# Kernel optimization log

Hardware: AMD Instinct MI355X
Metric: run time of the kernel (lower is better)

The kernel has to match this reference:

```python
import jax, jax.numpy as jnp
import numpy as np

LAYERS, BLOCKS = 10, 4
NL = LAYERS * BLOCKS
RC, DC, SC, EC, CLASSES, K = 32, 32, 256, 256, 256, 2
B, T = 8, 16384


def setup_inputs() -> dict:
    key = jax.random.key(0)
    ks = jax.random.split(key, 10)
    s = 0.1  # small init so tanh/sigmoid stay in informative range
    f32 = jnp.float32
    return {
        "x": jax.random.normal(ks[0], (B, CLASSES, T), dtype=f32),
        "w_in": jax.random.normal(ks[1], (RC, CLASSES, 1), dtype=f32) * s,
        "b_in": jnp.zeros((RC,), dtype=f32),
        "filt_w": jax.random.normal(ks[2], (NL, DC, RC, K), dtype=f32) * s,
        "filt_b": jnp.zeros((NL, DC), dtype=f32),
        "gate_w": jax.random.normal(ks[3], (NL, DC, RC, K), dtype=f32) * s,
        "gate_b": jnp.zeros((NL, DC), dtype=f32),
        "res_w": jax.random.normal(ks[4], (NL, RC, DC, K), dtype=f32) * s,
        "res_b": jnp.zeros((NL, RC), dtype=f32),
        "skip_w": jax.random.normal(ks[5], (NL, SC, DC, K), dtype=f32) * s,
        "skip_b": jnp.zeros((NL, SC), dtype=f32),
        "end1_w": jax.random.normal(ks[6], (EC, SC, 1), dtype=f32) * s,
        "end1_b": jnp.zeros((EC,), dtype=f32),
        "end2_w": jax.random.normal(ks[7], (CLASSES, EC, 1), dtype=f32) * s,
        "end2_b": jnp.zeros((CLASSES,), dtype=f32),
    }


def _causal_conv(x, w, b, d):
    # Equivalent to torch Conv1d(padding=d, dilation=d, k=2) followed by [:, :, :L]:
    # y[t] = w[..,0] @ x[t-d] + w[..,1] @ x[t]
    y = jax.lax.conv_general_dilated(
        x, w, window_strides=(1,), padding=[(d, 0)], rhs_dilation=(d,),
        dimension_numbers=("NCH", "OIH", "NCH"))
    return y + b[None, :, None]


def _conv1x1(x, w, b):
    return jnp.einsum("bct,oc->bot", x, w[:, :, 0]) + b[None, :, None]


def reference(x, w_in, b_in, filt_w, filt_b, gate_w, gate_b,
              res_w, res_b, skip_w, skip_b, end1_w, end1_b, end2_w, end2_b):
    h = _conv1x1(x, w_in, b_in)                      # [B, RC, T]
    skip = jnp.zeros((x.shape[0], SC, x.shape[2]), dtype=x.dtype)
    for i in range(NL):
        d = 2 ** (i % LAYERS)
        f = jnp.tanh(_causal_conv(h, filt_w[i], filt_b[i], d))
        g = jax.nn.sigmoid(_causal_conv(h, gate_w[i], gate_b[i], d))
        z = f * g                                    # [B, DC, T]
        skip = skip + _causal_conv(z, skip_w[i], skip_b[i], d)
        h = h + _causal_conv(z, res_w[i], res_b[i], d)
    out = jax.nn.relu(skip)
    out = jax.nn.relu(_conv1x1(out, end1_w, end1_b))
    out = _conv1x1(out, end2_w, end2_b)              # [B, CLASSES, T]
    n, c, l = out.shape
    return out.transpose(0, 2, 1).reshape(n * l, c)  # [B*T, CLASSES]
```

## Files before the change

### kernel.cpp

```cpp
#include <hip/hip_runtime.h>
#include <cstdint>
#include <cstddef>

#define T_LEN    16384
#define BATCH    8
#define BT       (BATCH * T_LEN)
#define NLAYERS  40

typedef unsigned short ushort_t;
typedef unsigned int   uint_t;
typedef __attribute__((ext_vector_type(8))) short    short8;
typedef __attribute__((ext_vector_type(4))) float    float4v;
typedef __attribute__((ext_vector_type(8))) _Float16 half8;

__device__ __forceinline__ ushort_t f2bf(float f) {
    union { float f; uint_t i; } v; v.f = f;
    uint_t r = (v.i + 0x7FFFu + ((v.i >> 16) & 1u)) >> 16;
    return (ushort_t)r;
}
__device__ __forceinline__ float fast_rcp(float x) {
#if __has_builtin(__builtin_amdgcn_rcpf)
    return __builtin_amdgcn_rcpf(x);
#else
    return 1.f / x;
#endif
}
__device__ __forceinline__ float tanh_fast(float x) {
    float e = __expf(2.f * x);
    return 1.f - 2.f * fast_rcp(e + 1.f);
}
__device__ __forceinline__ float sigmoid_fast(float x) {
    return fast_rcp(1.f + __expf(-x));
}
__device__ __forceinline__ float4v mfma16(short8 a, short8 b, float4v c) {
    return __builtin_amdgcn_mfma_f32_16x16x32_bf16(a, b, c, 0, 0, 0);
}

__global__ __launch_bounds__(256) void k_prep(
    const float* __restrict__ filt_w, const float* __restrict__ gate_w,
    const float* __restrict__ res_w,  const float* __restrict__ skip_w,
    const float* __restrict__ end1_w, const float* __restrict__ end2_w,
    const float* __restrict__ filt_b, const float* __restrict__ gate_b,
    const float* __restrict__ res_b,  const float* __restrict__ skip_b,
    const float* __restrict__ end1_b, const float* __restrict__ end2_b,
    ushort_t* __restrict__ wfgF, ushort_t* __restrict__ wrF,
    ushort_t* __restrict__ bsF,  ushort_t* __restrict__ e1F, ushort_t* __restrict__ e2F,
    float* __restrict__ bfg, float* __restrict__ brb, float* __restrict__ bsum,
    float* __restrict__ b1,  float* __restrict__ b2)
{
    const int gt = blockIdx.x * blockDim.x + threadIdx.x;
    const int gs = gridDim.x * blockDim.x;

    for (int e = gt; e < NLAYERS * 4 * 2 * 512; e += gs) {
        int j = e & 7, lane = (e >> 3) & 63, f = e >> 9;
        int ks = f & 1, nt = (f >> 1) & 3, i = f >> 3;
        int ln = lane & 15, q = lane >> 4, c = q * 8 + j;
        int o = (nt & 1) * 16 + ln;
        float v = (nt < 2) ? filt_w[((i * 32 + o) * 32 + c) * 2 + ks]
                           : gate_w[((i * 32 + o) * 32 + c) * 2 + ks];
        wfgF[e] = f2bf(v);
    }
    for (int e = gt; e < NLAYERS * 2 * 2 * 512; e += gs) {
        int j = e & 7, lane = (e >> 3) & 63, f = e >> 9;
        int ks = f & 1, nt = (f >> 1) & 1, i = f >> 2;
        int ln = lane & 15, q = lane >> 4, c = q * 8 + j;
        int o = nt * 16 + ln;
        wrF[e] = f2bf(res_w[((i * 32 + o) * 32 + c) * 2 + ks]);
    }
    for (int e = gt; e < 80 * 16 * 512; e += gs) {
        int j = e & 7, lane = (e >> 3) & 63, f = e >> 9;
        int nt = f & 15, ks80 = f >> 4;
        int i = ks80 >> 1, tap = ks80 & 1;
        int ln = lane & 15, q = lane >> 4, c = q * 8 + j;
        int o = nt * 16 + ln;
        bsF[e] = f2bf(skip_w[((i * 256 + o) * 32 + c) * 2 + tap]);
    }
    for (int e = gt; e < 8 * 16 * 512; e += gs) {
        int j = e & 7, lane = (e >> 3) & 63, f = e >> 9;
        int nt = f & 15, ks = f >> 4;
        int ln = lane & 15, q = lane >> 4;
        int k = ks * 32 + q * 8 + j;
        int o = nt * 16 + ln;
        e1F[e] = f2bf(end1_w[o * 256 + k]);
        e2F[e] = f2bf(end2_w[o * 256 + k]);
    }
    for (int e = gt; e < NLAYERS * 64; e += gs) {
        int i = e >> 6, c = e & 63;
        bfg[e] = (c < 32) ? filt_b[i * 32 + c] : gate_b[i * 32 + (c - 32)];
    }
    for (int e = gt; e < NLAYERS * 32; e += gs) {
        int i = e >> 5, c = e & 31;
        brb[e] = res_b[i * 32 + c];
    }
    for (int e = gt; e < 256; e += gs) {
        float s = 0.f;
        for (int i = 0; i < NLAYERS; ++i) s += skip_b[i * 256 + e];
        bsum[e] = s;
        b1[e] = end1_b[e];
        b2[e] = end2_b[e];
    }
}

__global__ __launch_bounds__(256) void k_input(
    const float* __restrict__ x, const float* __restrict__ w_in,
    const float* __restrict__ b_in, _Float16* __restrict__ h16)
{
    __shared__ __align__(16) float ws[256 * 32];
    for (int idx = threadIdx.x; idx < 256 * 32; idx += 256) {
        int o = idx >> 8, c = idx & 255;
        ws[c * 32 + o] = w_in[idx];
    }
    __syncthreads();
    const int bt = blockIdx.x * 256 + threadIdx.x;
    const float* xp = x + (size_t)(bt >> 14) * 256 * T_LEN + (bt & (T_LEN - 1));
    float acc[32];
#pragma unroll
    for (int o = 0; o < 32; ++o) acc[o] = b_in[o];
    for (int c = 0; c < 256; ++c) {
        float xv = xp[(size_t)c * T_LEN];
        const float4v* wr = (const float4v*)&ws[c * 32];
#pragma unroll
        for (int g = 0; g < 8; ++g) {
            float4v w4 = wr[g];
            acc[g * 4 + 0] += xv * w4[0];
            acc[g * 4 + 1] += xv * w4[1];
            acc[g * 4 + 2] += xv * w4[2];
            acc[g * 4 + 3] += xv * w4[3];
        }
    }
    half8* dst = (half8*)(h16 + (size_t)bt * 32);
#pragma unroll
    for (int g = 0; g < 4; ++g) {
        half8 v;
#pragma unroll
        for (int j = 0; j < 8; ++j) v[j] = (_Float16)acc[g * 8 + j];
        dst[g] = v;
    }
}

__global__ __launch_bounds__(256) void k_fg(
    const _Float16* __restrict__ h16, const ushort_t* __restrict__ wfgF,
    const float* __restrict__ bfg, ushort_t* __restrict__ zAll,
    int layer, int dil)
{
    const int w = threadIdx.x >> 6, lane = threadIdx.x & 63;
    const int ln = lane & 15, q = lane >> 4;
    const int bt0 = (blockIdx.x * 4 + w) * 16;
    const int m = bt0 + ln;
    const int koff = q * 8;

    short8 a0 = {0, 0, 0, 0, 0, 0, 0, 0}, a1;
    {
        half8 hv = *(const half8*)(h16 + (size_t)m * 32 + koff);
#pragma unroll
        for (int j = 0; j < 8; ++j) a1[j] = (short)f2bf((float)hv[j]);
    }
    if ((m & (T_LEN - 1)) >= dil) {
        half8 hv = *(const half8*)(h16 + (size_t)(m - dil) * 32 + koff);
#pragma unroll
        for (int j = 0; j < 8; ++j) a0[j] = (short)f2bf((float)hv[j]);
    }

    const short8* wf8 = (const short8*)wfgF;
    const float4v vzero = {0.f, 0.f, 0.f, 0.f};
    float4v acc[4];
#pragma unroll
    for (int nt = 0; nt < 4; ++nt) {
        float4v c = vzero;
        short8 b0 = wf8[(((size_t)layer * 4 + nt) * 2 + 0) * 64 + lane];
        short8 b1 = wf8[(((size_t)layer * 4 + nt) * 2 + 1) * 64 + lane];
        c = mfma16(a0, b0, c);
        c = mfma16(a1, b1, c);
        acc[nt] = c;
    }

    const float bF0 = bfg[layer * 64 + ln],      bF1 = bfg[layer * 64 + 16 + ln];
    const float bG0 = bfg[layer * 64 + 32 + ln], bG1 = bfg[layer * 64 + 48 + ln];
    ushort_t* zl = zAll + (size_t)layer * BT * 32;
#pragma unroll
    for (int r = 0; r < 4; ++r) {
        int row = bt0 + q * 4 + r;
        float z0 = tanh_fast(acc[0][r] + bF0) * sigmoid_fast(acc[2][r] + bG0);
        float z1 = tanh_fast(acc[1][r] + bF1) * sigmoid_fast(acc[3][r] + bG1);
        zl[(size_t)row * 32 + ln]      = f2bf(z0);
        zl[(size_t)row * 32 + 16 + ln] = f2bf(z1);
    }
}

__global__ __launch_bounds__(256) void k_res(
    _Float16* __restrict__ h16, const ushort_t* __restrict__ zAll,
    const ushort_t* __restrict__ wrF, const float* __restrict__ brb,
    int layer, int dil)
{
    __shared__ float lds[4][16 * 35];
    const int w = threadIdx.x >> 6, lane = threadIdx.x & 63;
    const int ln = lane & 15, q = lane >> 4;
    const int bt0 = (blockIdx.x * 4 + w) * 16;
    const int m = bt0 + ln;
    const int koff = q * 8;

    const ushort_t* zl = zAll + (size_t)layer * BT * 32;
    short8 a0 = {0, 0, 0, 0, 0, 0, 0, 0};
    if ((m & (T_LEN - 1)) >= dil)
        a0 = *(const short8*)(zl + (size_t)(m - dil) * 32 + koff);
    short8 a1 = *(const short8*)(zl + (size_t)m * 32 + koff);

    const short8* wr8 = (const short8*)wrF;
    const float4v vzero = {0.f, 0.f, 0.f, 0.f};
    float4v acc0 = vzero, acc1 = vzero;
    acc0 = mfma16(a0, wr8[(((size_t)layer * 2 + 0) * 2 + 0) * 64 + lane], acc0);
    acc0 = mfma16(a1, wr8[(((size_t)layer * 2 + 0) * 2 + 1) * 64 + lane], acc0);
    acc1 = mfma16(a0, wr8[(((size_t)layer * 2 + 1) * 2 + 0) * 64 + lane], acc1);
    acc1 = mfma16(a1, wr8[(((size_t)layer * 2 + 1) * 2 + 1) * 64 + lane], acc1);

    const float b0 = brb[layer * 32 + ln], b1 = brb[layer * 32 + 16 + ln];
#pragma unroll
    for (int r = 0; r < 4; ++r) {
        lds[w][(q * 4 + r) * 35 + ln]      = acc0[r] + b0;
        lds[w][(q * 4 + r) * 35 + 16 + ln] = acc1[r] + b1;
    }
    __syncthreads();
    const int p = lane & 15, g8 = lane >> 4;
    _Float16* hp = h16 + (size_t)(bt0 + p) * 32 + g8 * 8;
    half8 hv = *(const half8*)hp;
#pragma unroll
    for (int j = 0; j < 8; ++j)
        hv[j] = (_Float16)((float)hv[j] + lds[w][p * 35 + g8 * 8 + j]);
    *(half8*)hp = hv;
}

__global__ __launch_bounds__(256) void k_skip_gemm(
    const ushort_t* __restrict__ zAll, const ushort_t* __restrict__ bsF,
    const float* __restrict__ bsum, ushort_t* __restrict__ skipbuf)
{
    __shared__ __align__(16) ushort_t ldsB[8 * 512];
    const int tid = threadIdx.x;
    const int w = tid >> 6, lane = tid & 63;
    const int wR = w >> 1, wC = w & 1;
    const int ln = lane & 15, q = lane >> 4, koff = q * 8;
    const int mBase = blockIdx.x * 128 + wR * 64;
    const int nBase = blockIdx.y * 128 + wC * 64;

    const float4v vzero = {0.f, 0.f, 0.f, 0.f};
    const short8 zero8 = {0, 0, 0, 0, 0, 0, 0, 0};
    float4v acc[4][4];
#pragma unroll
    for (int mt = 0; mt < 4; ++mt)
#pragma unroll
        for (int nt = 0; nt < 4; ++nt) acc[mt][nt] = vzero;

    for (int ks = 0; ks < 80; ++ks) {
        const short8* gsrc = (const short8*)bsF + ((size_t)ks * 16 + blockIdx.y * 8) * 64;
        short8 s0 = gsrc[tid];
        short8 s1 = gsrc[tid + 256];

        const int i = ks >> 1, tap = ks & 1;
        const int dil = 1 << (i % 10);
        const ushort_t* zl = zAll + (size_t)i * BT * 32;
        short8 a[4];
#pragma unroll
        for (int mt = 0; mt < 4; ++mt) {
            int m = mBase + mt * 16 + ln;
            if (tap) {
                a[mt] = *(const short8*)(zl + (size_t)m * 32 + koff);
            } else if ((m & (T_LEN - 1)) >= dil) {
                a[mt] = *(const short8*)(zl + (size_t)(m - dil) * 32 + koff);
            } else {
                a[mt] = zero8;
            }
        }
        ((short8*)ldsB)[tid] = s0;
        ((short8*)ldsB)[tid + 256] = s1;
        __syncthreads();
        short8 bfr[4];
#pragma unroll
        for (int nt = 0; nt < 4; ++nt)
            bfr[nt] = ((const short8*)ldsB)[(wC * 4 + nt) * 64 + lane];
#pragma unroll
        for (int mt = 0; mt < 4; ++mt)
#pragma unroll
            for (int nt = 0; nt < 4; ++nt)
                acc[mt][nt] = mfma16(a[mt], bfr[nt], acc[mt][nt]);
        __syncthreads();
    }

#pragma unroll
    for (int nt = 0; nt < 4; ++nt) {
        const int n = nBase + nt * 16 + ln;
        const float bias = bsum[n];
#pragma unroll
        for (int mt = 0; mt < 4; ++mt)
#pragma unroll
            for (int r = 0; r < 4; ++r) {
                int row = mBase + mt * 16 + q * 4 + r;
                float v = fmaxf(acc[mt][nt][r] + bias, 0.f);
                skipbuf[(size_t)row * 256 + n] = f2bf(v);
            }
    }
}

__global__ __launch_bounds__(256) void k_gemm256(
    const ushort_t* __restrict__ A, const ushort_t* __restrict__ BF,
    const float* __restrict__ bias, ushort_t* __restrict__ outB,
    float* __restrict__ outF, int relu)
{
    __shared__ __align__(16) ushort_t ldsB[8 * 512];
    const int tid = threadIdx.x;
    const int w = tid >> 6, lane = tid & 63;
    const int wR = w >> 1, wC = w & 1;
    const int ln = lane & 15, q = lane >> 4, koff = q * 8;
    const int mBase = blockIdx.x * 128 + wR * 64;
    const int nBase = blockIdx.y * 128 + wC * 64;

    const float4v vzero = {0.f, 0.f, 0.f, 0.f};
    float4v acc[4][4];
#pragma unroll
    for (int mt = 0; mt < 4; ++mt)
#pragma unroll
        for (int nt = 0; nt < 4; ++nt) acc[mt][nt] = vzero;

    for (int ks = 0; ks < 8; ++ks) {
        const short8* gsrc = (const short8*)BF + ((size_t)ks * 16 + blockIdx.y * 8) * 64;
        short8 s0 = gsrc[tid];
        short8 s1 = gsrc[tid + 256];
        short8 a[4];
#pragma unroll
        for (int mt = 0; mt < 4; ++mt) {
            int m = mBase + mt * 16 + ln;
            a[mt] = *(const short8*)(A + (size_t)m * 256 + ks * 32 + koff);
        }
        ((short8*)ldsB)[tid] = s0;
        ((short8*)ldsB)[tid + 256] = s1;
        __syncthreads();
        short8 bfr[4];
#pragma unroll
        for (int nt = 0; nt < 4; ++nt)
            bfr[nt] = ((const short8*)ldsB)[(wC * 4 + nt) * 64 + lane];
#pragma unroll
        for (int mt = 0; mt < 4; ++mt)
#pragma unroll
            for (int nt = 0; nt < 4; ++nt)
                acc[mt][nt] = mfma16(a[mt], bfr[nt], acc[mt][nt]);
        __syncthreads();
    }

#pragma unroll
    for (int nt = 0; nt < 4; ++nt) {
        const int n = nBase + nt * 16 + ln;
        const float b = bias[n];
#pragma unroll
        for (int mt = 0; mt < 4; ++mt)
#pragma unroll
            for (int r = 0; r < 4; ++r) {
                int row = mBase + mt * 16 + q * 4 + r;
                float v = acc[mt][nt][r] + b;
                if (relu) v = fmaxf(v, 0.f);
                if (outF) outF[(size_t)row * 256 + n] = v;
                else      outB[(size_t)row * 256 + n] = f2bf(v);
            }
    }
}

extern "C" void kernel_launch(void* const* d_in, const int* in_sizes, int n_in,
                              void* d_out, int out_size, void* d_ws, size_t ws_size,
                              hipStream_t stream)
{
    (void)in_sizes; (void)n_in; (void)out_size; (void)ws_size;
    const float* x      = (const float*)d_in[0];
    const float* w_in   = (const float*)d_in[1];
    const float* b_in   = (const float*)d_in[2];
    const float* filt_w = (const float*)d_in[3];
    const float* filt_b = (const float*)d_in[4];
    const float* gate_w = (const float*)d_in[5];
    const float* gate_b = (const float*)d_in[6];
    const float* res_w  = (const float*)d_in[7];
    const float* res_b  = (const float*)d_in[8];
    const float* skip_w = (const float*)d_in[9];
    const float* skip_b = (const float*)d_in[10];
    const float* end1_w = (const float*)d_in[11];
    const float* end1_b = (const float*)d_in[12];
    const float* end2_w = (const float*)d_in[13];
    const float* end2_b = (const float*)d_in[14];

    char* ws = (char*)d_ws;
    size_t off = 0;
    auto alloc = [&](size_t bytes) {
        char* p = ws + off;
        off += (bytes + 255) & ~(size_t)255;
        return p;
    };
    ushort_t* zAll    = (ushort_t*)alloc((size_t)NLAYERS * BT * 32 * 2);
    ushort_t* skipbuf = (ushort_t*)alloc((size_t)BT * 256 * 2);
    _Float16* h16     = (_Float16*)alloc((size_t)BT * 32 * 2);
    ushort_t* wfgF    = (ushort_t*)alloc((size_t)NLAYERS * 4 * 2 * 512 * 2);
    ushort_t* wrF     = (ushort_t*)alloc((size_t)NLAYERS * 2 * 2 * 512 * 2);
    ushort_t* bsF     = (ushort_t*)alloc((size_t)80 * 16 * 512 * 2);
    ushort_t* e1F     = (ushort_t*)alloc((size_t)8 * 16 * 512 * 2);
    ushort_t* e2F     = (ushort_t*)alloc((size_t)8 * 16 * 512 * 2);
    float* bfg  = (float*)alloc((size_t)NLAYERS * 64 * 4);
    float* brb  = (float*)alloc((size_t)NLAYERS * 32 * 4);
    float* bsum = (float*)alloc(256 * 4);
    float* b1   = (float*)alloc(256 * 4);
    float* b2   = (float*)alloc(256 * 4);
    ushort_t* out1 = zAll;

    k_prep<<<256, 256, 0, stream>>>(filt_w, gate_w, res_w, skip_w, end1_w, end2_w,
                                    filt_b, gate_b, res_b, skip_b, end1_b, end2_b,
                                    wfgF, wrF, bsF, e1F, e2F, bfg, brb, bsum, b1, b2);
    k_input<<<BT / 256, 256, 0, stream>>>(x, w_in, b_in, h16);
    for (int i = 0; i < NLAYERS; ++i) {
        int dil = 1 << (i % 10);
        k_fg<<<BT / 64, 256, 0, stream>>>(h16, wfgF, bfg, zAll, i, dil);
        k_res<<<BT / 64, 256, 0, stream>>>(h16, zAll, wrF, brb, i, dil);
    }
    dim3 g3(BT / 128, 2);
    k_skip_gemm<<<g3, 256, 0, stream>>>(zAll, bsF, bsum, skipbuf);
    k_gemm256<<<g3, 256, 0, stream>>>(skipbuf, e1F, b1, out1, nullptr, 1);
    k_gemm256<<<g3, 256, 0, stream>>>(out1, e2F, b2, nullptr, (float*)d_out, 0);
}
```

Baseline: 1.318 ms.

## Fuse residual update with next layer's gate, widen skip GEMM, fuse end convs

Merges each layer's residual conv with the following layer's filter/gate conv into one kernel. It recomputes the residual at t-dilN from the current z so the next layer's causal taps are ready without an extra launch, and ping-pongs h between two buffers. The skip GEMM now covers all 256 output columns per block and both taps per iteration. The two end 1x1 convs are fused through LDS so the intermediate activation never goes to global memory. This halves the per-layer launches and cuts intermediate traffic, at the cost of duplicated residual MFMAs, extra z reads and larger LDS use per block.

```diff
diff --git a/kernel.cpp b/kernel.cpp
--- a/kernel.cpp
+++ b/kernel.cpp
@@ -187,59 +187,114 @@
     }
 }
 
-__global__ __launch_bounds__(256) void k_res(
-    _Float16* __restrict__ h16, const ushort_t* __restrict__ zAll,
+__global__ __launch_bounds__(256) void k_resfg(
+    const _Float16* __restrict__ hin, _Float16* __restrict__ hout,
+    ushort_t* __restrict__ zAll,
     const ushort_t* __restrict__ wrF, const float* __restrict__ brb,
-    int layer, int dil)
-{
-    __shared__ float lds[4][16 * 35];
+    const ushort_t* __restrict__ wfgF, const float* __restrict__ bfg,
+    int layer, int dil, int dilN)
+{
+    __shared__ float lds[4][2][2][16 * 33];
     const int w = threadIdx.x >> 6, lane = threadIdx.x & 63;
     const int ln = lane & 15, q = lane >> 4;
-    const int bt0 = (blockIdx.x * 4 + w) * 16;
-    const int m = bt0 + ln;
     const int koff = q * 8;
-
+    const int bt0 = (blockIdx.x * 4 + w) * 32;
     const ushort_t* zl = zAll + (size_t)layer * BT * 32;
-    short8 a0 = {0, 0, 0, 0, 0, 0, 0, 0};
-    if ((m & (T_LEN - 1)) >= dil)
-        a0 = *(const short8*)(zl + (size_t)(m - dil) * 32 + koff);
-    short8 a1 = *(const short8*)(zl + (size_t)m * 32 + koff);
-
+    ushort_t* zo = zAll + (size_t)(layer + 1) * BT * 32;
     const short8* wr8 = (const short8*)wrF;
+    const short8* wf8 = (const short8*)wfgF;
     const float4v vzero = {0.f, 0.f, 0.f, 0.f};
-    float4v acc0 = vzero, acc1 = vzero;
-    acc0 = mfma16(a0, wr8[(((size_t)layer * 2 + 0) * 2 + 0) * 64 + lane], acc0);
-    acc0 = mfma16(a1, wr8[(((size_t)layer * 2 + 0) * 2 + 1) * 64 + lane], acc0);
-    acc1 = mfma16(a0, wr8[(((size_t)layer * 2 + 1) * 2 + 0) * 64 + lane], acc1);
-    acc1 = mfma16(a1, wr8[(((size_t)layer * 2 + 1) * 2 + 1) * 64 + lane], acc1);
-
-    const float b0 = brb[layer * 32 + ln], b1 = brb[layer * 32 + 16 + ln];
-#pragma unroll
-    for (int r = 0; r < 4; ++r) {
-        lds[w][(q * 4 + r) * 35 + ln]      = acc0[r] + b0;
-        lds[w][(q * 4 + r) * 35 + 16 + ln] = acc1[r] + b1;
+    const short8 zero8 = {0, 0, 0, 0, 0, 0, 0, 0};
+
+    const short8 rb00 = wr8[(((size_t)layer * 2 + 0) * 2 + 0) * 64 + lane];
+    const short8 rb01 = wr8[(((size_t)layer * 2 + 0) * 2 + 1) * 64 + lane];
+    const short8 rb10 = wr8[(((size_t)layer * 2 + 1) * 2 + 0) * 64 + lane];
+    const short8 rb11 = wr8[(((size_t)layer * 2 + 1) * 2 + 1) * 64 + lane];
+    const float br0 = brb[layer * 32 + ln], br1 = brb[layer * 32 + 16 + ln];
+
+#pragma unroll
+    for (int mt = 0; mt < 2; ++mt) {
+        const int mb = bt0 + mt * 16;
+        const int m = mb + ln;
+        const int tln = m & (T_LEN - 1);
+        short8 a1 = *(const short8*)(zl + (size_t)m * 32 + koff);
+        short8 a0 = (tln >= dil) ? *(const short8*)(zl + (size_t)(m - dil) * 32 + koff) : zero8;
+        float4v c0 = mfma16(a0, rb00, vzero); c0 = mfma16(a1, rb01, c0);
+        float4v c1 = mfma16(a0, rb10, vzero); c1 = mfma16(a1, rb11, c1);
+        short8 p1 = (tln >= dilN)       ? *(const short8*)(zl + (size_t)(m - dilN) * 32 + koff)       : zero8;
+        short8 p0 = (tln >= dilN + dil) ? *(const short8*)(zl + (size_t)(m - dilN - dil) * 32 + koff) : zero8;
+        float4v d0 = mfma16(p0, rb00, vzero); d0 = mfma16(p1, rb01, d0);
+        float4v d1 = mfma16(p0, rb10, vzero); d1 = mfma16(p1, rb11, d1);
+
+        float* t0 = &lds[w][mt][0][0];
+        float* t1 = &lds[w][mt][1][0];
+#pragma unroll
+        for (int r = 0; r < 4; ++r) {
+            int row = q * 4 + r;
+            int grow = mb + row;
+            int tr = grow & (T_LEN - 1);
+            float h0a = (float)hin[(size_t)grow * 32 + ln];
+            float h0b = (float)hin[(size_t)grow * 32 + 16 + ln];
+            t0[row * 33 + ln]      = c0[r] + br0 + h0a;
+            t0[row * 33 + 16 + ln] = c1[r] + br1 + h0b;
+            float hpa = 0.f, hpb = 0.f;
+            if (tr >= dilN) {
+                hpa = (float)hin[(size_t)(grow - dilN) * 32 + ln]      + d0[r] + br0;
+                hpb = (float)hin[(size_t)(grow - dilN) * 32 + 16 + ln] + d1[r] + br1;
+            }
+            t1[row * 33 + ln]      = hpa;
+            t1[row * 33 + 16 + ln] = hpb;
+        }
     }
     __syncthreads();
-    const int p = lane & 15, g8 = lane >> 4;
-    _Float16* hp = h16 + (size_t)(bt0 + p) * 32 + g8 * 8;
-    half8 hv = *(const half8*)hp;
-#pragma unroll
-    for (int j = 0; j < 8; ++j)
-        hv[j] = (_Float16)((float)hv[j] + lds[w][p * 35 + g8 * 8 + j]);
-    *(half8*)hp = hv;
-}
-
-__global__ __launch_bounds__(256) void k_skip_gemm(
+
+    const int L1 = layer + 1;
+    const float bF0 = bfg[L1 * 64 + ln],      bF1 = bfg[L1 * 64 + 16 + ln];
+    const float bG0 = bfg[L1 * 64 + 32 + ln], bG1 = bfg[L1 * 64 + 48 + ln];
+#pragma unroll
+    for (int mt = 0; mt < 2; ++mt) {
+        const int mb = bt0 + mt * 16;
+        const float* t0 = &lds[w][mt][0][0];
+        const float* t1 = &lds[w][mt][1][0];
+        short8 fa1, fa0;
+#pragma unroll
+        for (int j = 0; j < 8; ++j) {
+            fa1[j] = (short)f2bf(t0[ln * 33 + koff + j]);
+            fa0[j] = (short)f2bf(t1[ln * 33 + koff + j]);
+        }
+        float4v acc[4];
+#pragma unroll
+        for (int nt = 0; nt < 4; ++nt) {
+            float4v c = vzero;
+            c = mfma16(fa0, wf8[(((size_t)L1 * 4 + nt) * 2 + 0) * 64 + lane], c);
+            c = mfma16(fa1, wf8[(((size_t)L1 * 4 + nt) * 2 + 1) * 64 + lane], c);
+            acc[nt] = c;
+        }
+#pragma unroll
+        for (int r = 0; r < 4; ++r) {
+            int row = mb + q * 4 + r;
+            float z0 = tanh_fast(acc[0][r] + bF0) * sigmoid_fast(acc[2][r] + bG0);
+            float z1 = tanh_fast(acc[1][r] + bF1) * sigmoid_fast(acc[3][r] + bG1);
+            zo[(size_t)row * 32 + ln]      = f2bf(z0);
+            zo[(size_t)row * 32 + 16 + ln] = f2bf(z1);
+        }
+        half8 hv;
+#pragma unroll
+        for (int j = 0; j < 8; ++j) hv[j] = (_Float16)t0[ln * 33 + q * 8 + j];
+        *(half8*)(hout + (size_t)(mb + ln) * 32 + q * 8) = hv;
+    }
+}
+
+__global__ __launch_bounds__(512) void k_skip_gemm(
     const ushort_t* __restrict__ zAll, const ushort_t* __restrict__ bsF,
     const float* __restrict__ bsum, ushort_t* __restrict__ skipbuf)
 {
-    __shared__ __align__(16) ushort_t ldsB[8 * 512];
+    __shared__ __align__(16) ushort_t ldsB[32 * 512];
     const int tid = threadIdx.x;
     const int w = tid >> 6, lane = tid & 63;
-    const int wR = w >> 1, wC = w & 1;
+    const int wR = w >> 2, wC = w & 3;
     const int ln = lane & 15, q = lane >> 4, koff = q * 8;
     const int mBase = blockIdx.x * 128 + wR * 64;
-    const int nBase = blockIdx.y * 128 + wC * 64;
 
     const float4v vzero = {0.f, 0.f, 0.f, 0.f};
     const short8 zero8 = {0, 0, 0, 0, 0, 0, 0, 0};
@@ -249,44 +304,42 @@
 #pragma unroll
         for (int nt = 0; nt < 4; ++nt) acc[mt][nt] = vzero;
 
-    for (int ks = 0; ks < 80; ++ks) {
-        const short8* gsrc = (const short8*)bsF + ((size_t)ks * 16 + blockIdx.y * 8) * 64;
-        short8 s0 = gsrc[tid];
-        short8 s1 = gsrc[tid + 256];
-
-        const int i = ks >> 1, tap = ks & 1;
+    short8* lb = (short8*)ldsB;
+    for (int i = 0; i < NLAYERS; ++i) {
+        const short8* gsrc = (const short8*)(bsF + (size_t)i * 32 * 512);
+        short8 s0 = gsrc[tid], s1 = gsrc[tid + 512], s2 = gsrc[tid + 1024], s3 = gsrc[tid + 1536];
+
         const int dil = 1 << (i % 10);
         const ushort_t* zl = zAll + (size_t)i * BT * 32;
-        short8 a[4];
+        short8 a1[4], a0[4];
 #pragma unroll
         for (int mt = 0; mt < 4; ++mt) {
             int m = mBase + mt * 16 + ln;
-            if (tap) {
-                a[mt] = *(const short8*)(zl + (size_t)m * 32 + koff);
-            } else if ((m & (T_LEN - 1)) >= dil) {
-                a[mt] = *(const short8*)(zl + (size_t)(m - dil) * 32 + koff);
-            } else {
-                a[mt] = zero8;
+            int tln = m & (T_LEN - 1);
+            a1[mt] = *(const short8*)(zl + (size_t)m * 32 + koff);
+            a0[mt] = (tln >= dil) ? *(const short8*)(zl + (size_t)(m - dil) * 32 + koff) : zero8;
+        }
+        lb[tid] = s0; lb[tid + 512] = s1; lb[tid + 1024] = s2; lb[tid + 1536] = s3;
+        __syncthreads();
+        short8 b0[4], b1[4];
+#pragma unroll
+        for (int nt = 0; nt < 4; ++nt) {
+            b0[nt] = lb[(wC * 4 + nt) * 64 + lane];
+            b1[nt] = lb[(16 + wC * 4 + nt) * 64 + lane];
+        }
+#pragma unroll
+        for (int mt = 0; mt < 4; ++mt)
+#pragma unroll
+            for (int nt = 0; nt < 4; ++nt) {
+                acc[mt][nt] = mfma16(a0[mt], b0[nt], acc[mt][nt]);
+                acc[mt][nt] = mfma16(a1[mt], b1[nt], acc[mt][nt]);
             }
-        }
-        ((short8*)ldsB)[tid] = s0;
-        ((short8*)ldsB)[tid + 256] = s1;
         __syncthreads();
-        short8 bfr[4];
-#pragma unroll
-        for (int nt = 0; nt < 4; ++nt)
-            bfr[nt] = ((const short8*)ldsB)[(wC * 4 + nt) * 64 + lane];
-#pragma unroll
-        for (int mt = 0; mt < 4; ++mt)
-#pragma unroll
-            for (int nt = 0; nt < 4; ++nt)
-                acc[mt][nt] = mfma16(a[mt], bfr[nt], acc[mt][nt]);
-        __syncthreads();
     }
 
 #pragma unroll
     for (int nt = 0; nt < 4; ++nt) {
-        const int n = nBase + nt * 16 + ln;
+        const int n = wC * 64 + nt * 16 + ln;
         const float bias = bsum[n];
 #pragma unroll
         for (int mt = 0; mt < 4; ++mt)
@@ -299,18 +352,18 @@
     }
 }
 
-__global__ __launch_bounds__(256) void k_gemm256(
-    const ushort_t* __restrict__ A, const ushort_t* __restrict__ BF,
-    const float* __restrict__ bias, ushort_t* __restrict__ outB,
-    float* __restrict__ outF, int relu)
-{
-    __shared__ __align__(16) ushort_t ldsB[8 * 512];
+__global__ __launch_bounds__(512) void k_end(
+    const ushort_t* __restrict__ skipbuf, const ushort_t* __restrict__ e1F,
+    const ushort_t* __restrict__ e2F, const float* __restrict__ b1,
+    const float* __restrict__ b2, float* __restrict__ out)
+{
+    __shared__ __align__(16) ushort_t ldsS[16 * 512];
+    __shared__ __align__(16) ushort_t ldsA[64 * 512];
     const int tid = threadIdx.x;
     const int w = tid >> 6, lane = tid & 63;
-    const int wR = w >> 1, wC = w & 1;
+    const int wR = w >> 2, wC = w & 3;
     const int ln = lane & 15, q = lane >> 4, koff = q * 8;
     const int mBase = blockIdx.x * 128 + wR * 64;
-    const int nBase = blockIdx.y * 128 + wC * 64;
 
     const float4v vzero = {0.f, 0.f, 0.f, 0.f};
     float4v acc[4][4];
@@ -319,23 +372,21 @@
 #pragma unroll
         for (int nt = 0; nt < 4; ++nt) acc[mt][nt] = vzero;
 
+    short8* ls = (short8*)ldsS;
     for (int ks = 0; ks < 8; ++ks) {
-        const short8* gsrc = (const short8*)BF + ((size_t)ks * 16 + blockIdx.y * 8) * 64;
-        short8 s0 = gsrc[tid];
-        short8 s1 = gsrc[tid + 256];
+        const short8* gsrc = (const short8*)(e1F + (size_t)ks * 16 * 512);
+        short8 s0 = gsrc[tid], s1 = gsrc[tid + 512];
         short8 a[4];
 #pragma unroll
         for (int mt = 0; mt < 4; ++mt) {
             int m = mBase + mt * 16 + ln;
-            a[mt] = *(const short8*)(A + (size_t)m * 256 + ks * 32 + koff);
-        }
-        ((short8*)ldsB)[tid] = s0;
-        ((short8*)ldsB)[tid + 256] = s1;
+            a[mt] = *(const short8*)(skipbuf + (size_t)m * 256 + ks * 32 + koff);
+        }
+        ls[tid] = s0; ls[tid + 512] = s1;
         __syncthreads();
         short8 bfr[4];
 #pragma unroll
-        for (int nt = 0; nt < 4; ++nt)
-            bfr[nt] = ((const short8*)ldsB)[(wC * 4 + nt) * 64 + lane];
+        for (int nt = 0; nt < 4; ++nt) bfr[nt] = ls[(wC * 4 + nt) * 64 + lane];
 #pragma unroll
         for (int mt = 0; mt < 4; ++mt)
 #pragma unroll
@@ -343,20 +394,58 @@
                 acc[mt][nt] = mfma16(a[mt], bfr[nt], acc[mt][nt]);
         __syncthreads();
     }
-
 #pragma unroll
     for (int nt = 0; nt < 4; ++nt) {
-        const int n = nBase + nt * 16 + ln;
-        const float b = bias[n];
+        const int col = wC * 64 + nt * 16 + ln;
+        const float bb = b1[col];
+        const int fk = col >> 5;
+        const int l2hi = ((col >> 3) & 3) << 4;
+        const int j = col & 7;
+#pragma unroll
+        for (int mt = 0; mt < 4; ++mt) {
+            const int fr = wR * 4 + mt;
+#pragma unroll
+            for (int r = 0; r < 4; ++r) {
+                int lane2 = (q * 4 + r) | l2hi;
+                float v = fmaxf(acc[mt][nt][r] + bb, 0.f);
+                ldsA[((fr * 8 + fk) * 64 + lane2) * 8 + j] = f2bf(v);
+            }
+        }
+    }
+    __syncthreads();
+#pragma unroll
+    for (int mt = 0; mt < 4; ++mt)
+#pragma unroll
+        for (int nt = 0; nt < 4; ++nt) acc[mt][nt] = vzero;
+    for (int ks = 0; ks < 8; ++ks) {
+        const short8* gsrc = (const short8*)(e2F + (size_t)ks * 16 * 512);
+        short8 s0 = gsrc[tid], s1 = gsrc[tid + 512];
+        short8 a[4];
+#pragma unroll
+        for (int mt = 0; mt < 4; ++mt)
+            a[mt] = ((const short8*)ldsA)[((size_t)(wR * 4 + mt) * 8 + ks) * 64 + lane];
+        ls[tid] = s0; ls[tid + 512] = s1;
+        __syncthreads();
+        short8 bfr[4];
+#pragma unroll
+        for (int nt = 0; nt < 4; ++nt) bfr[nt] = ls[(wC * 4 + nt) * 64 + lane];
+#pragma unroll
+        for (int mt = 0; mt < 4; ++mt)
+#pragma unroll
+            for (int nt = 0; nt < 4; ++nt)
+                acc[mt][nt] = mfma16(a[mt], bfr[nt], acc[mt][nt]);
+        __syncthreads();
+    }
+#pragma unroll
+    for (int nt = 0; nt < 4; ++nt) {
+        const int n = wC * 64 + nt * 16 + ln;
+        const float bb = b2[n];
 #pragma unroll
         for (int mt = 0; mt < 4; ++mt)
 #pragma unroll
             for (int r = 0; r < 4; ++r) {
                 int row = mBase + mt * 16 + q * 4 + r;
-                float v = acc[mt][nt][r] + b;
-                if (relu) v = fmaxf(v, 0.f);
-                if (outF) outF[(size_t)row * 256 + n] = v;
-                else      outB[(size_t)row * 256 + n] = f2bf(v);
+                out[(size_t)row * 256 + n] = acc[mt][nt][r] + bb;
             }
     }
 }
@@ -391,7 +480,8 @@
     };
     ushort_t* zAll    = (ushort_t*)alloc((size_t)NLAYERS * BT * 32 * 2);
     ushort_t* skipbuf = (ushort_t*)alloc((size_t)BT * 256 * 2);
-    _Float16* h16     = (_Float16*)alloc((size_t)BT * 32 * 2);
+    _Float16* hA      = (_Float16*)skipbuf;
+    _Float16* hB      = (_Float16*)(skipbuf + (size_t)BT * 32);
     ushort_t* wfgF    = (ushort_t*)alloc((size_t)NLAYERS * 4 * 2 * 512 * 2);
     ushort_t* wrF     = (ushort_t*)alloc((size_t)NLAYERS * 2 * 2 * 512 * 2);
     ushort_t* bsF     = (ushort_t*)alloc((size_t)80 * 16 * 512 * 2);
@@ -402,19 +492,20 @@
     float* bsum = (float*)alloc(256 * 4);
     float* b1   = (float*)alloc(256 * 4);
     float* b2   = (float*)alloc(256 * 4);
-    ushort_t* out1 = zAll;
 
     k_prep<<<256, 256, 0, stream>>>(filt_w, gate_w, res_w, skip_w, end1_w, end2_w,
                                     filt_b, gate_b, res_b, skip_b, end1_b, end2_b,
                                     wfgF, wrF, bsF, e1F, e2F, bfg, brb, bsum, b1, b2);
-    k_input<<<BT / 256, 256, 0, stream>>>(x, w_in, b_in, h16);
-    for (int i = 0; i < NLAYERS; ++i) {
-        int dil = 1 << (i % 10);
-        k_fg<<<BT / 64, 256, 0, stream>>>(h16, wfgF, bfg, zAll, i, dil);
-        k_res<<<BT / 64, 256, 0, stream>>>(h16, zAll, wrF, brb, i, dil);
-    }
-    dim3 g3(BT / 128, 2);
-    k_skip_gemm<<<g3, 256, 0, stream>>>(zAll, bsF, bsum, skipbuf);
-    k_gemm256<<<g3, 256, 0, stream>>>(skipbuf, e1F, b1, out1, nullptr, 1);
-    k_gemm256<<<g3, 256, 0, stream>>>(out1, e2F, b2, nullptr, (float*)d_out, 0);
-}
+    k_input<<<BT / 256, 256, 0, stream>>>(x, w_in, b_in, hA);
+    k_fg<<<BT / 64, 256, 0, stream>>>(hA, wfgF, bfg, zAll, 0, 1);
+    for (int i = 0; i < NLAYERS - 1; ++i) {
+        const _Float16* hin = (i & 1) ? hB : hA;
+        _Float16*       ho  = (i & 1) ? hA : hB;
+        int dil  = 1 << (i % 10);
+        int dilN = 1 << ((i + 1) % 10);
+        k_resfg<<<BT / 128, 256, 0, stream>>>(hin, ho, zAll, wrF, brb, wfgF, bfg,
+                                              i, dil, dilN);
+    }
+    k_skip_gemm<<<BT / 128, 512, 0, stream>>>(zAll, bsF, bsum, skipbuf);
+    k_end<<<BT / 128, 512, 0, stream>>>(skipbuf, e1F, e2F, b1, b2, (float*)d_out);
+}
```

Measured after the change: 1.252 ms. 1.05x faster.
